# Optimization experiments

Measured on AMD Instinct MI355X. Metric: run time of the kernel, lower is better.

Reference implementation:

```python
import jax, jax.numpy as jnp
import numpy as np

N_NODES = 100000
N_EDGES = 600000
N_GRAPHS = 64
BN_EPS = 1e-5


def setup_inputs() -> dict:
    key = jax.random.key(0)
    ks = jax.random.split(key, 32)
    inp = {
        "x": jax.random.normal(ks[0], (N_NODES, 128), dtype=jnp.float32),
        "edge_index": jax.random.randint(ks[1], (2, N_EDGES), 0, N_NODES, dtype=jnp.int64),
        "batch": jnp.sort(jax.random.randint(ks[2], (N_NODES,), 0, N_GRAPHS, dtype=jnp.int64)),
    }
    dims = [(128, 64, 64), (64, 64, 64), (64, 64, 96)]  # (in, hid, out) per GIN layer
    ki = 3
    for i, (d_in, d_hid, d_out) in enumerate(dims):
        inp[f"l{i}_w1"] = jax.random.normal(ks[ki], (d_in, d_hid), dtype=jnp.float32) * 0.05; ki += 1
        inp[f"l{i}_b1"] = jnp.zeros((d_hid,), dtype=jnp.float32)
        inp[f"l{i}_w2"] = jax.random.normal(ks[ki], (d_hid, d_out), dtype=jnp.float32) * 0.05; ki += 1
        inp[f"l{i}_b2"] = jnp.zeros((d_out,), dtype=jnp.float32)
        inp[f"bn{i}_g"] = jax.random.uniform(ks[ki], (d_out,), minval=0.5, maxval=1.5, dtype=jnp.float32); ki += 1
        inp[f"bn{i}_b"] = jax.random.normal(ks[ki], (d_out,), dtype=jnp.float32) * 0.05; ki += 1
        inp[f"bn{i}_m"] = jax.random.normal(ks[ki], (d_out,), dtype=jnp.float32) * 0.05; ki += 1
        inp[f"bn{i}_v"] = jax.random.uniform(ks[ki], (d_out,), minval=0.5, maxval=1.5, dtype=jnp.float32); ki += 1
    return inp


def _gin_layer(x, src, dst, w1, b1, w2, b2, g, bb, m, v):
    # GINConv (eps=0): h_i = MLP(x_i + sum_{j: j->i} x_j)
    aggr = jax.ops.segment_sum(x[src], dst, num_segments=N_NODES)
    h = x + aggr
    h = jax.nn.relu(h @ w1 + b1) @ w2 + b2
    # eval-mode BatchNorm1d + ReLU
    h = (h - m) * jax.lax.rsqrt(v + BN_EPS) * g + bb
    return jax.nn.relu(h)


def reference(x, edge_index, batch,
              l0_w1, l0_b1, l0_w2, l0_b2, bn0_g, bn0_b, bn0_m, bn0_v,
              l1_w1, l1_b1, l1_w2, l1_b2, bn1_g, bn1_b, bn1_m, bn1_v,
              l2_w1, l2_b1, l2_w2, l2_b2, bn2_g, bn2_b, bn2_m, bn2_v):
    src, dst = edge_index[0], edge_index[1]
    h = _gin_layer(x, src, dst, l0_w1, l0_b1, l0_w2, l0_b2, bn0_g, bn0_b, bn0_m, bn0_v)
    h = _gin_layer(h, src, dst, l1_w1, l1_b1, l1_w2, l1_b2, bn1_g, bn1_b, bn1_m, bn1_v)
    h = _gin_layer(h, src, dst, l2_w1, l2_b1, l2_w2, l2_b2, bn2_g, bn2_b, bn2_m, bn2_v)
    # global mean pool over graphs
    sums = jax.ops.segment_sum(h, batch, num_segments=N_GRAPHS)
    counts = jax.ops.segment_sum(jnp.ones((h.shape[0],), dtype=h.dtype), batch, num_segments=N_GRAPHS)
    return sums / jnp.maximum(counts, 1.0)[:, None]
```

## Files before the change

kernel.cpp:

```cpp
#include <hip/hip_runtime.h>

#define N_NODES 100000
#define N_GRAPHS 64
#define N_EDGES 600000
#define BN_EPS 1e-5f

typedef unsigned short bf16_t;

__device__ __forceinline__ unsigned short f2bf(float f) {
    unsigned int u = __float_as_uint(f);
    u += 0x7FFF + ((u >> 16) & 1);
    return (unsigned short)(u >> 16);
}
__device__ __forceinline__ float4 bf2f4(uint2 p) {
    float4 r;
    r.x = __uint_as_float(p.x << 16);
    r.y = __uint_as_float(p.x & 0xFFFF0000u);
    r.z = __uint_as_float(p.y << 16);
    r.w = __uint_as_float(p.y & 0xFFFF0000u);
    return r;
}
__device__ __forceinline__ uint2 pack4(float a, float b, float c, float d) {
    uint2 p;
    p.x = (unsigned)f2bf(a) | ((unsigned)f2bf(b) << 16);
    p.y = (unsigned)f2bf(c) | ((unsigned)f2bf(d) << 16);
    return p;
}

__global__ void deg_hist_kernel(const int* __restrict__ dst,
                                int* __restrict__ deg, int n_edges) {
    int e = blockIdx.x * blockDim.x + threadIdx.x;
    if (e < n_edges) atomicAdd(&deg[dst[e]], 1);
}

__global__ void scan1_kernel(const int* __restrict__ deg, int* __restrict__ excl,
                             int* __restrict__ partials, int n) {
    __shared__ int s[1024];
    int i = blockIdx.x * 1024 + threadIdx.x;
    int v = (i < n) ? deg[i] : 0;
    s[threadIdx.x] = v;
    __syncthreads();
    for (int off = 1; off < 1024; off <<= 1) {
        int t = (threadIdx.x >= (unsigned)off) ? s[threadIdx.x - off] : 0;
        __syncthreads();
        s[threadIdx.x] += t;
        __syncthreads();
    }
    if (i < n) excl[i] = s[threadIdx.x] - v;
    if (threadIdx.x == 1023) partials[blockIdx.x] = s[1023];
}

__global__ void scan2_kernel(int* partials, int nb) {
    __shared__ int s[128];
    int t = threadIdx.x;
    int v = (t < nb) ? partials[t] : 0;
    s[t] = v;
    __syncthreads();
    for (int off = 1; off < 128; off <<= 1) {
        int u = (t >= off) ? s[t - off] : 0;
        __syncthreads();
        s[t] += u;
        __syncthreads();
    }
    if (t < nb) partials[t] = s[t] - v;
}

__global__ void scan3_kernel(int* __restrict__ rowptr, const int* __restrict__ partials,
                             int n, int total) {
    int i = blockIdx.x * blockDim.x + threadIdx.x;
    if (i < n) rowptr[i] += partials[i >> 10];
    else if (i == n) rowptr[n] = total;
}

__global__ void fill_bounds_kernel(const int* __restrict__ src, const int* __restrict__ dst,
                                   const int* __restrict__ rowptr, int* __restrict__ cursor,
                                   int* __restrict__ eids, const int* __restrict__ batch,
                                   int* __restrict__ gstart, int n_edges, int n_nodes) {
    int e = blockIdx.x * blockDim.x + threadIdx.x;
    if (e < n_edges) {
        int t = dst[e];
        int pos = rowptr[t] + atomicAdd(&cursor[t], 1);
        eids[pos] = src[e];
    }
    if (e < n_nodes) {
        if (e == 0) {
            for (int g = 0; g <= batch[0]; ++g) gstart[g] = 0;
        } else {
            int b0 = batch[e - 1], b1 = batch[e];
            for (int g = b0 + 1; g <= b1; ++g) gstart[g] = e;
        }
        if (e == n_nodes - 1) {
            for (int g = batch[e] + 1; g <= N_GRAPHS; ++g) gstart[g] = n_nodes;
        }
    }
}

struct LayerPrep {
    const float *w1, *w2, *b2, *g, *bb, *m, *v;
    float *w1T, *w2sT, *bias2;
    int DIN, DOUT;
};
struct PrepAll { LayerPrep l[3]; };

__global__ void prep_all_kernel(PrepAll pa, int* __restrict__ deg,
                                int* __restrict__ cursor) {
    LayerPrep P = pa.l[blockIdx.y];
    int i = blockIdx.x * blockDim.x + threadIdx.x;
    if (blockIdx.y == 0) {
        int stride = gridDim.x * blockDim.x;
        for (int k = i; k < N_NODES; k += stride) { deg[k] = 0; cursor[k] = 0; }
    }
    if (i < 64 * P.DIN) {
        int j = i / P.DIN, k = i % P.DIN;
        P.w1T[i] = P.w1[k * 64 + j];
    }
    int i2 = i - 64 * P.DIN;
    if (i2 >= 0 && i2 < P.DOUT * 64) {
        int c = i2 / 64, j = i2 % 64;
        float s = P.g[c] * rsqrtf(P.v[c] + BN_EPS);
        P.w2sT[i2] = P.w2[j * P.DOUT + c] * s;
    }
    int i3 = i2 - P.DOUT * 64;
    if (i3 >= 0 && i3 < P.DOUT) {
        float s = P.g[i3] * rsqrtf(P.v[i3] + BN_EPS);
        P.bias2[i3] = (P.b2[i3] - P.m[i3]) * s + P.bb[i3];
    }
}

__global__ __launch_bounds__(256)
void pre_gemm_kernel(const float* __restrict__ x, const float* __restrict__ w1T,
                     bf16_t* __restrict__ y, int n_nodes) {
    __shared__ float w1s[64 * 128];
    const int tid = threadIdx.x;
    const long base = (long)blockIdx.x * 128;

    const float4* gw1 = (const float4*)w1T;
    for (int i4 = tid; i4 < 16 * 128; i4 += 256) {
        int row = i4 >> 5, k4 = i4 & 31;
        *(float4*)&w1s[row * 128 + ((k4 ^ ((row >> 2) & 7)) << 2)] = gw1[i4];
    }
    __syncthreads();

    const int jg = tid & 15, ng = tid >> 4, xw = jg & 7;
    const float* wp = &w1s[(jg * 4) * 128];
    const float4* xv = (const float4*)x;
    long r[8];
    #pragma unroll
    for (int i = 0; i < 8; ++i) {
        long rr = base + ng * 8 + i;
        r[i] = (rr < n_nodes) ? rr : (n_nodes - 1);
    }
    float acc[8][4] = {};
    #pragma unroll 2
    for (int k4 = 0; k4 < 32; ++k4) {
        const int ko = (k4 ^ xw) << 2;
        float4 w0 = *(const float4*)&wp[0 * 128 + ko];
        float4 w1v = *(const float4*)&wp[1 * 128 + ko];
        float4 w2v = *(const float4*)&wp[2 * 128 + ko];
        float4 w3v = *(const float4*)&wp[3 * 128 + ko];
        #pragma unroll
        for (int i = 0; i < 8; ++i) {
            float4 a = xv[r[i] * 32 + k4];
            acc[i][0] = fmaf(a.x, w0.x, fmaf(a.y, w0.y, fmaf(a.z, w0.z, fmaf(a.w, w0.w, acc[i][0]))));
            acc[i][1] = fmaf(a.x, w1v.x, fmaf(a.y, w1v.y, fmaf(a.z, w1v.z, fmaf(a.w, w1v.w, acc[i][1]))));
            acc[i][2] = fmaf(a.x, w2v.x, fmaf(a.y, w2v.y, fmaf(a.z, w2v.z, fmaf(a.w, w2v.w, acc[i][2]))));
            acc[i][3] = fmaf(a.x, w3v.x, fmaf(a.y, w3v.y, fmaf(a.z, w3v.z, fmaf(a.w, w3v.w, acc[i][3]))));
        }
    }
    #pragma unroll
    for (int i = 0; i < 8; ++i) {
        long n = base + ng * 8 + i;
        if (n < n_nodes) {
            *(uint2*)(y + n * 64 + jg * 4) = pack4(acc[i][0], acc[i][1], acc[i][2], acc[i][3]);
        }
    }
}

__global__ __launch_bounds__(256)
void gather64_kernel(const bf16_t* __restrict__ y, const int* __restrict__ rowptr,
                     const int* __restrict__ eids, const float* __restrict__ b1,
                     float* __restrict__ t, int n_nodes) {
    int node = blockIdx.x * 16 + (threadIdx.x >> 4);
    if (node >= n_nodes) return;
    int f4 = threadIdx.x & 15;
    const uint2* yv = (const uint2*)y;
    float4 acc = bf2f4(yv[(long)node * 16 + f4]);
    int b = rowptr[node], e = rowptr[node + 1];
    int i = b;
    for (; i + 3 < e; i += 4) {
        int s0 = eids[i], s1 = eids[i + 1], s2 = eids[i + 2], s3 = eids[i + 3];
        uint2 q0 = yv[(long)s0 * 16 + f4];
        uint2 q1 = yv[(long)s1 * 16 + f4];
        uint2 q2 = yv[(long)s2 * 16 + f4];
        uint2 q3 = yv[(long)s3 * 16 + f4];
        float4 r0 = bf2f4(q0), r1 = bf2f4(q1), r2 = bf2f4(q2), r3 = bf2f4(q3);
        acc.x += (r0.x + r1.x) + (r2.x + r3.x);
        acc.y += (r0.y + r1.y) + (r2.y + r3.y);
        acc.z += (r0.z + r1.z) + (r2.z + r3.z);
        acc.w += (r0.w + r1.w) + (r2.w + r3.w);
    }
    for (; i < e; ++i) {
        int s = eids[i];
        float4 r = bf2f4(yv[(long)s * 16 + f4]);
        acc.x += r.x; acc.y += r.y; acc.z += r.z; acc.w += r.w;
    }
    float4 bv = ((const float4*)b1)[f4];
    float4 o;
    o.x = fmaxf(acc.x + bv.x, 0.0f);
    o.y = fmaxf(acc.y + bv.y, 0.0f);
    o.z = fmaxf(acc.z + bv.z, 0.0f);
    o.w = fmaxf(acc.w + bv.w, 0.0f);
    ((float4*)t)[(long)node * 16 + f4] = o;
}

__global__ __launch_bounds__(256)
void fused_mid_kernel(const float* __restrict__ t, const float* __restrict__ w2sT,
                      const float* __restrict__ bias2, const float* __restrict__ w1nT,
                      bf16_t* __restrict__ ynext, int n_nodes) {
    constexpr int SS = 68;
    __shared__ float sT[64 * SS];
    __shared__ float wbuf[64 * 64];
    const int tid = threadIdx.x;
    const long base = (long)blockIdx.x * 64;

    const float4* gw2 = (const float4*)w2sT;
    for (int i4 = tid; i4 < 16 * 64; i4 += 256) {
        int row = i4 >> 4, k4 = i4 & 15;
        *(float4*)&wbuf[row * 64 + ((k4 ^ ((row >> 2) & 7)) << 2)] = gw2[i4];
    }
    __syncthreads();

    const int jg = tid & 15, ng = tid >> 4, xw = jg & 7;
    const float4* tv = (const float4*)(t + base * 64);

    float h[4][4];
    {
        const float* wp = &wbuf[(jg * 4) * 64];
        float acc[4][4] = {};
        #pragma unroll 4
        for (int k4 = 0; k4 < 16; ++k4) {
            const int ko = (k4 ^ xw) << 2;
            float4 w0 = *(const float4*)&wp[0 * 64 + ko];
            float4 w1v = *(const float4*)&wp[1 * 64 + ko];
            float4 w2v = *(const float4*)&wp[2 * 64 + ko];
            float4 w3v = *(const float4*)&wp[3 * 64 + ko];
            #pragma unroll
            for (int i = 0; i < 4; ++i) {
                float4 a = tv[(ng * 4 + i) * 16 + k4];
                acc[i][0] = fmaf(a.x, w0.x, fmaf(a.y, w0.y, fmaf(a.z, w0.z, fmaf(a.w, w0.w, acc[i][0]))));
                acc[i][1] = fmaf(a.x, w1v.x, fmaf(a.y, w1v.y, fmaf(a.z, w1v.z, fmaf(a.w, w1v.w, acc[i][1]))));
                acc[i][2] = fmaf(a.x, w2v.x, fmaf(a.y, w2v.y, fmaf(a.z, w2v.z, fmaf(a.w, w2v.w, acc[i][2]))));
                acc[i][3] = fmaf(a.x, w3v.x, fmaf(a.y, w3v.y, fmaf(a.z, w3v.z, fmaf(a.w, w3v.w, acc[i][3]))));
            }
        }
        float4 bv = *(const float4*)&bias2[jg * 4];
        #pragma unroll
        for (int i = 0; i < 4; ++i) {
            h[i][0] = fmaxf(acc[i][0] + bv.x, 0.0f);
            h[i][1] = fmaxf(acc[i][1] + bv.y, 0.0f);
            h[i][2] = fmaxf(acc[i][2] + bv.z, 0.0f);
            h[i][3] = fmaxf(acc[i][3] + bv.w, 0.0f);
        }
    }
    __syncthreads();

    #pragma unroll
    for (int i = 0; i < 4; ++i) {
        float4 hv = {h[i][0], h[i][1], h[i][2], h[i][3]};
        *(float4*)&sT[(ng * 4 + i) * SS + jg * 4] = hv;
    }
    const float4* gw1n = (const float4*)w1nT;
    for (int i4 = tid; i4 < 16 * 64; i4 += 256) {
        int row = i4 >> 4, k4 = i4 & 15;
        *(float4*)&wbuf[row * 64 + ((k4 ^ ((row >> 2) & 7)) << 2)] = gw1n[i4];
    }
    __syncthreads();

    {
        const float* ap = &sT[(ng * 4) * SS];
        const float* wp = &wbuf[(jg * 4) * 64];
        float acc[4][4] = {};
        #pragma unroll 4
        for (int k4 = 0; k4 < 16; ++k4) {
            const int ko = (k4 ^ xw) << 2;
            float4 w0 = *(const float4*)&wp[0 * 64 + ko];
            float4 w1v = *(const float4*)&wp[1 * 64 + ko];
            float4 w2v = *(const float4*)&wp[2 * 64 + ko];
            float4 w3v = *(const float4*)&wp[3 * 64 + ko];
            #pragma unroll
            for (int i = 0; i < 4; ++i) {
                float4 a = *(const float4*)&ap[i * SS + k4 * 4];
                acc[i][0] = fmaf(a.x, w0.x, fmaf(a.y, w0.y, fmaf(a.z, w0.z, fmaf(a.w, w0.w, acc[i][0]))));
                acc[i][1] = fmaf(a.x, w1v.x, fmaf(a.y, w1v.y, fmaf(a.z, w1v.z, fmaf(a.w, w1v.w, acc[i][1]))));
                acc[i][2] = fmaf(a.x, w2v.x, fmaf(a.y, w2v.y, fmaf(a.z, w2v.z, fmaf(a.w, w2v.w, acc[i][2]))));
                acc[i][3] = fmaf(a.x, w3v.x, fmaf(a.y, w3v.y, fmaf(a.z, w3v.z, fmaf(a.w, w3v.w, acc[i][3]))));
            }
        }
        #pragma unroll
        for (int i = 0; i < 4; ++i) {
            long n = base + ng * 4 + i;
            if (n < n_nodes) {
                *(uint2*)(ynext + n * 64 + jg * 4) = pack4(acc[i][0], acc[i][1], acc[i][2], acc[i][3]);
            }
        }
    }
}

__global__ __launch_bounds__(256)
void fused_final_kernel(const float* __restrict__ t, const float* __restrict__ w2sT,
                        const float* __restrict__ bias2, float* __restrict__ out,
                        int n_nodes) {
    constexpr int CPT = 6;
    __shared__ float w2s[96 * 64];
    const int tid = threadIdx.x;
    const long base = (long)blockIdx.x * 64;

    const float4* gw2 = (const float4*)w2sT;
    for (int i4 = tid; i4 < 96 * 16; i4 += 256) {
        int row = i4 >> 4, k4 = i4 & 15;
        *(float4*)&w2s[row * 64 + ((k4 ^ ((row / CPT) & 7)) << 2)] = gw2[i4];
    }
    __syncthreads();

    const int cg_ = tid & 15, ng = tid >> 4, xw = cg_ & 7;
    const float4* tv = (const float4*)(t + base * 64);
    const float* wp = &w2s[(cg_ * CPT) * 64];
    float acc[4][CPT] = {};
    #pragma unroll 4
    for (int k4 = 0; k4 < 16; ++k4) {
        const int ko = (k4 ^ xw) << 2;
        float4 wv[CPT];
        #pragma unroll
        for (int c = 0; c < CPT; ++c) wv[c] = *(const float4*)&wp[c * 64 + ko];
        #pragma unroll
        for (int i = 0; i < 4; ++i) {
            float4 h = tv[(ng * 4 + i) * 16 + k4];
            #pragma unroll
            for (int c = 0; c < CPT; ++c)
                acc[i][c] = fmaf(h.x, wv[c].x, fmaf(h.y, wv[c].y, fmaf(h.z, wv[c].z, fmaf(h.w, wv[c].w, acc[i][c]))));
        }
    }
    float bv[CPT];
    #pragma unroll
    for (int c = 0; c < CPT; ++c) bv[c] = bias2[cg_ * CPT + c];
    #pragma unroll
    for (int i = 0; i < 4; ++i) {
        long n = base + ng * 4 + i;
        if (n < n_nodes) {
            float* op = out + n * 96 + cg_ * CPT;
            #pragma unroll
            for (int c = 0; c < CPT; ++c) op[c] = fmaxf(acc[i][c] + bv[c], 0.0f);
        }
    }
}

#define POOL_SPLIT 16
__global__ __launch_bounds__(192)
void pool_seg_kernel(const float* __restrict__ h, const int* __restrict__ gstart,
                     float* __restrict__ part) {
    int g = blockIdx.x >> 4;
    int s = blockIdx.x & 15;
    int lo = gstart[g], hi = gstart[g + 1];
    int len = hi - lo;
    int seg = (len + POOL_SPLIT - 1) / POOL_SPLIT;
    int a = lo + s * seg;
    int b = a + seg; if (b > hi) b = hi;

    int f4 = threadIdx.x % 24;
    int chain = threadIdx.x / 24;
    const float4* hv = (const float4*)h;
    float4 acc = {0.0f, 0.0f, 0.0f, 0.0f};
    for (int n = a + chain; n < b; n += 8) {
        float4 v = hv[(long)n * 24 + f4];
        acc.x += v.x; acc.y += v.y; acc.z += v.z; acc.w += v.w;
    }
    __shared__ float4 red[8][24];
    red[chain][f4] = acc;
    __syncthreads();
    if (threadIdx.x < 24) {
        float4 t = red[0][threadIdx.x];
        #pragma unroll
        for (int c = 1; c < 8; ++c) {
            float4 r = red[c][threadIdx.x];
            t.x += r.x; t.y += r.y; t.z += r.z; t.w += r.w;
        }
        *(float4*)&part[((long)blockIdx.x) * 96 + threadIdx.x * 4] = t;
    }
}

__global__ void finalize_kernel(const float* __restrict__ part,
                                const int* __restrict__ gstart,
                                float* __restrict__ out) {
    int i = blockIdx.x * blockDim.x + threadIdx.x;
    if (i >= N_GRAPHS * 96) return;
    int g = i / 96, c = i - g * 96;
    float s = 0.0f;
    #pragma unroll
    for (int k = 0; k < POOL_SPLIT; ++k) s += part[((long)g * POOL_SPLIT + k) * 96 + c];
    float cnt = (float)(gstart[g + 1] - gstart[g]);
    out[i] = s / fmaxf(cnt, 1.0f);
}

static inline int cdiv_l(long a, int b) { return (int)((a + b - 1) / b); }

extern "C" void kernel_launch(void* const* d_in, const int* in_sizes, int n_in,
                              void* d_out, int out_size, void* d_ws, size_t ws_size,
                              hipStream_t stream) {
    const float* x     = (const float*)d_in[0];
    const int*   ei    = (const int*)d_in[1];
    const int*   src   = ei;
    const int*   dst   = ei + N_EDGES;
    const int*   batch = (const int*)d_in[2];

    const float* P[3][8];
    int p = 3;
    for (int l = 0; l < 3; ++l)
        for (int q = 0; q < 8; ++q)
            P[l][q] = (const float*)d_in[p++];

    const long NP = N_NODES + 128;
    char* wsb   = (char*)d_ws;
    bf16_t* yA  = (bf16_t*)wsb;
    bf16_t* yB  = yA + NP * 64;
    float* gB   = (float*)(yB + NP * 64);
    float* h2   = gB + NP * 64;
    float* q    = h2 + NP * 96;
    float* w1T[3], *w2sT[3], *bias2[3];
    for (int l = 0; l < 3; ++l) {
        w1T[l] = q;   q += 64 * 128;
        w2sT[l] = q;  q += 96 * 64;
        bias2[l] = q; q += 96;
    }
    float* part   = q;
    int* gstart   = (int*)(part + N_GRAPHS * POOL_SPLIT * 96);
    int* deg      = gstart + 72;
    int* cursor   = deg + N_NODES;
    int* partials = cursor + N_NODES;
    int* rowptr   = partials + 128;
    int* eids     = rowptr + (N_NODES + 1);

    const int B = 256;
    const int DIN[3]  = {128, 64, 64};
    const int DOUT[3] = {64, 64, 96};

    PrepAll pa;
    for (int l = 0; l < 3; ++l) {
        pa.l[l].w1 = P[l][0]; pa.l[l].w2 = P[l][2]; pa.l[l].b2 = P[l][3];
        pa.l[l].g = P[l][4];  pa.l[l].bb = P[l][5]; pa.l[l].m = P[l][6];
        pa.l[l].v = P[l][7];
        pa.l[l].w1T = w1T[l]; pa.l[l].w2sT = w2sT[l]; pa.l[l].bias2 = bias2[l];
        pa.l[l].DIN = DIN[l]; pa.l[l].DOUT = DOUT[l];
    }
    dim3 pgrid(cdiv_l(64 * 128 + 96 * 64 + 96, B), 3);
    prep_all_kernel<<<pgrid, B, 0, stream>>>(pa, deg, cursor);

    deg_hist_kernel<<<cdiv_l(N_EDGES, B), B, 0, stream>>>(dst, deg, N_EDGES);
    int nblk = cdiv_l(N_NODES, 1024);
    scan1_kernel<<<nblk, 1024, 0, stream>>>(deg, rowptr, partials, N_NODES);
    scan2_kernel<<<1, 128, 0, stream>>>(partials, nblk);
    scan3_kernel<<<cdiv_l(N_NODES + 1, B), B, 0, stream>>>(rowptr, partials, N_NODES, N_EDGES);
    fill_bounds_kernel<<<cdiv_l(N_EDGES, B), B, 0, stream>>>(
        src, dst, rowptr, cursor, eids, batch, gstart, N_EDGES, N_NODES);

    const int ntiles = cdiv_l(N_NODES, 64);
    const int ngather = cdiv_l(N_NODES, 16);

    pre_gemm_kernel<<<cdiv_l(N_NODES, 128), 256, 0, stream>>>(x, w1T[0], yA, N_NODES);
    gather64_kernel<<<ngather, 256, 0, stream>>>(yA, rowptr, eids, P[0][1], gB, N_NODES);
    fused_mid_kernel<<<ntiles, 256, 0, stream>>>(
        gB, w2sT[0], bias2[0], w1T[1], yB, N_NODES);
    gather64_kernel<<<ngather, 256, 0, stream>>>(yB, rowptr, eids, P[1][1], gB, N_NODES);
    fused_mid_kernel<<<ntiles, 256, 0, stream>>>(
        gB, w2sT[1], bias2[1], w1T[2], yA, N_NODES);
    gather64_kernel<<<ngather, 256, 0, stream>>>(yA, rowptr, eids, P[2][1], gB, N_NODES);
    fused_final_kernel<<<ntiles, 256, 0, stream>>>(
        gB, w2sT[2], bias2[2], h2, N_NODES);

    pool_seg_kernel<<<N_GRAPHS * POOL_SPLIT, 192, 0, stream>>>(h2, gstart, part);
    finalize_kernel<<<cdiv_l(N_GRAPHS * 96, B), B, 0, stream>>>(
        part, gstart, (float*)d_out);
}
```

Baseline: 396.3 us.

## Fuse neighbor gather into per-layer MLP kernels via shared-memory tiles

Removes the standalone gather kernels. Each fused MLP kernel now aggregates its 64-node tile's neighbor features straight into shared memory, then runs the GEMMs from there. This drops the fp32 intermediate buffer write and read and three kernel launches per forward. The trade-off is that each block does irregular gather work before its GEMM, so per-block latency and load imbalance rise. The first pre-GEMM also shrinks to 64 rows per block, giving more blocks.

After: 406.0 us. 1.02x slower.

```diff
diff --git a/kernel.cpp b/kernel.cpp
--- a/kernel.cpp
+++ b/kernel.cpp
@@ -132,7 +132,7 @@
                      bf16_t* __restrict__ y, int n_nodes) {
     __shared__ float w1s[64 * 128];
     const int tid = threadIdx.x;
-    const long base = (long)blockIdx.x * 128;
+    const long base = (long)blockIdx.x * 64;
 
     const float4* gw1 = (const float4*)w1T;
     for (int i4 = tid; i4 < 16 * 128; i4 += 256) {
@@ -144,14 +144,14 @@
     const int jg = tid & 15, ng = tid >> 4, xw = jg & 7;
     const float* wp = &w1s[(jg * 4) * 128];
     const float4* xv = (const float4*)x;
-    long r[8];
-    #pragma unroll
-    for (int i = 0; i < 8; ++i) {
-        long rr = base + ng * 8 + i;
+    long r[4];
+    #pragma unroll
+    for (int i = 0; i < 4; ++i) {
+        long rr = base + ng * 4 + i;
         r[i] = (rr < n_nodes) ? rr : (n_nodes - 1);
     }
-    float acc[8][4] = {};
-    #pragma unroll 2
+    float acc[4][4] = {};
+    #pragma unroll 4
     for (int k4 = 0; k4 < 32; ++k4) {
         const int ko = (k4 ^ xw) << 2;
         float4 w0 = *(const float4*)&wp[0 * 128 + ko];
@@ -159,7 +159,7 @@
         float4 w2v = *(const float4*)&wp[2 * 128 + ko];
         float4 w3v = *(const float4*)&wp[3 * 128 + ko];
         #pragma unroll
-        for (int i = 0; i < 8; ++i) {
+        for (int i = 0; i < 4; ++i) {
             float4 a = xv[r[i] * 32 + k4];
             acc[i][0] = fmaf(a.x, w0.x, fmaf(a.y, w0.y, fmaf(a.z, w0.z, fmaf(a.w, w0.w, acc[i][0]))));
             acc[i][1] = fmaf(a.x, w1v.x, fmaf(a.y, w1v.y, fmaf(a.z, w1v.z, fmaf(a.w, w1v.w, acc[i][1]))));
@@ -168,56 +168,67 @@
         }
     }
     #pragma unroll
-    for (int i = 0; i < 8; ++i) {
-        long n = base + ng * 8 + i;
+    for (int i = 0; i < 4; ++i) {
+        long n = base + ng * 4 + i;
         if (n < n_nodes) {
             *(uint2*)(y + n * 64 + jg * 4) = pack4(acc[i][0], acc[i][1], acc[i][2], acc[i][3]);
         }
     }
 }
 
+#define SS 68
+__device__ __forceinline__ void gather_tile_lds(const bf16_t* __restrict__ y,
+                                                const int* __restrict__ rowptr,
+                                                const int* __restrict__ eids,
+                                                const float* __restrict__ b1,
+                                                float* sT, long base, int n_nodes,
+                                                int tid) {
+    const uint2* yv = (const uint2*)y;
+    const int f4 = tid & 15;
+    const int gidx = tid >> 4;
+    const float4 bv = ((const float4*)b1)[f4];
+    #pragma unroll
+    for (int pass = 0; pass < 4; ++pass) {
+        int nl = pass * 16 + gidx;
+        long node = base + nl;
+        float4 acc = {0.0f, 0.0f, 0.0f, 0.0f};
+        if (node < n_nodes) {
+            acc = bf2f4(yv[node * 16 + f4]);
+            int b = rowptr[node], e = rowptr[node + 1];
+            int i = b;
+            for (; i + 3 < e; i += 4) {
+                int s0 = eids[i], s1 = eids[i + 1], s2 = eids[i + 2], s3 = eids[i + 3];
+                uint2 q0 = yv[(long)s0 * 16 + f4];
+                uint2 q1 = yv[(long)s1 * 16 + f4];
+                uint2 q2 = yv[(long)s2 * 16 + f4];
+                uint2 q3 = yv[(long)s3 * 16 + f4];
+                float4 r0 = bf2f4(q0), r1 = bf2f4(q1), r2 = bf2f4(q2), r3 = bf2f4(q3);
+                acc.x += (r0.x + r1.x) + (r2.x + r3.x);
+                acc.y += (r0.y + r1.y) + (r2.y + r3.y);
+                acc.z += (r0.z + r1.z) + (r2.z + r3.z);
+                acc.w += (r0.w + r1.w) + (r2.w + r3.w);
+            }
+            for (; i < e; ++i) {
+                int s = eids[i];
+                float4 r = bf2f4(yv[(long)s * 16 + f4]);
+                acc.x += r.x; acc.y += r.y; acc.z += r.z; acc.w += r.w;
+            }
+        }
+        float4 o;
+        o.x = fmaxf(acc.x + bv.x, 0.0f);
+        o.y = fmaxf(acc.y + bv.y, 0.0f);
+        o.z = fmaxf(acc.z + bv.z, 0.0f);
+        o.w = fmaxf(acc.w + bv.w, 0.0f);
+        *(float4*)&sT[nl * SS + f4 * 4] = o;
+    }
+}
+
 __global__ __launch_bounds__(256)
-void gather64_kernel(const bf16_t* __restrict__ y, const int* __restrict__ rowptr,
-                     const int* __restrict__ eids, const float* __restrict__ b1,
-                     float* __restrict__ t, int n_nodes) {
-    int node = blockIdx.x * 16 + (threadIdx.x >> 4);
-    if (node >= n_nodes) return;
-    int f4 = threadIdx.x & 15;
-    const uint2* yv = (const uint2*)y;
-    float4 acc = bf2f4(yv[(long)node * 16 + f4]);
-    int b = rowptr[node], e = rowptr[node + 1];
-    int i = b;
-    for (; i + 3 < e; i += 4) {
-        int s0 = eids[i], s1 = eids[i + 1], s2 = eids[i + 2], s3 = eids[i + 3];
-        uint2 q0 = yv[(long)s0 * 16 + f4];
-        uint2 q1 = yv[(long)s1 * 16 + f4];
-        uint2 q2 = yv[(long)s2 * 16 + f4];
-        uint2 q3 = yv[(long)s3 * 16 + f4];
-        float4 r0 = bf2f4(q0), r1 = bf2f4(q1), r2 = bf2f4(q2), r3 = bf2f4(q3);
-        acc.x += (r0.x + r1.x) + (r2.x + r3.x);
-        acc.y += (r0.y + r1.y) + (r2.y + r3.y);
-        acc.z += (r0.z + r1.z) + (r2.z + r3.z);
-        acc.w += (r0.w + r1.w) + (r2.w + r3.w);
-    }
-    for (; i < e; ++i) {
-        int s = eids[i];
-        float4 r = bf2f4(yv[(long)s * 16 + f4]);
-        acc.x += r.x; acc.y += r.y; acc.z += r.z; acc.w += r.w;
-    }
-    float4 bv = ((const float4*)b1)[f4];
-    float4 o;
-    o.x = fmaxf(acc.x + bv.x, 0.0f);
-    o.y = fmaxf(acc.y + bv.y, 0.0f);
-    o.z = fmaxf(acc.z + bv.z, 0.0f);
-    o.w = fmaxf(acc.w + bv.w, 0.0f);
-    ((float4*)t)[(long)node * 16 + f4] = o;
-}
-
-__global__ __launch_bounds__(256)
-void fused_mid_kernel(const float* __restrict__ t, const float* __restrict__ w2sT,
-                      const float* __restrict__ bias2, const float* __restrict__ w1nT,
-                      bf16_t* __restrict__ ynext, int n_nodes) {
-    constexpr int SS = 68;
+void fused_mid_kernel(const bf16_t* __restrict__ y, const int* __restrict__ rowptr,
+                      const int* __restrict__ eids, const float* __restrict__ b1,
+                      const float* __restrict__ w2sT, const float* __restrict__ bias2,
+                      const float* __restrict__ w1nT, bf16_t* __restrict__ ynext,
+                      int n_nodes) {
     __shared__ float sT[64 * SS];
     __shared__ float wbuf[64 * 64];
     const int tid = threadIdx.x;
@@ -228,54 +239,12 @@
         int row = i4 >> 4, k4 = i4 & 15;
         *(float4*)&wbuf[row * 64 + ((k4 ^ ((row >> 2) & 7)) << 2)] = gw2[i4];
     }
+    gather_tile_lds(y, rowptr, eids, b1, sT, base, n_nodes, tid);
     __syncthreads();
 
     const int jg = tid & 15, ng = tid >> 4, xw = jg & 7;
-    const float4* tv = (const float4*)(t + base * 64);
 
     float h[4][4];
-    {
-        const float* wp = &wbuf[(jg * 4) * 64];
-        float acc[4][4] = {};
-        #pragma unroll 4
-        for (int k4 = 0; k4 < 16; ++k4) {
-            const int ko = (k4 ^ xw) << 2;
-            float4 w0 = *(const float4*)&wp[0 * 64 + ko];
-            float4 w1v = *(const float4*)&wp[1 * 64 + ko];
-            float4 w2v = *(const float4*)&wp[2 * 64 + ko];
-            float4 w3v = *(const float4*)&wp[3 * 64 + ko];
-            #pragma unroll
-            for (int i = 0; i < 4; ++i) {
-                float4 a = tv[(ng * 4 + i) * 16 + k4];
-                acc[i][0] = fmaf(a.x, w0.x, fmaf(a.y, w0.y, fmaf(a.z, w0.z, fmaf(a.w, w0.w, acc[i][0]))));
-                acc[i][1] = fmaf(a.x, w1v.x, fmaf(a.y, w1v.y, fmaf(a.z, w1v.z, fmaf(a.w, w1v.w, acc[i][1]))));
-                acc[i][2] = fmaf(a.x, w2v.x, fmaf(a.y, w2v.y, fmaf(a.z, w2v.z, fmaf(a.w, w2v.w, acc[i][2]))));
-                acc[i][3] = fmaf(a.x, w3v.x, fmaf(a.y, w3v.y, fmaf(a.z, w3v.z, fmaf(a.w, w3v.w, acc[i][3]))));
-            }
-        }
-        float4 bv = *(const float4*)&bias2[jg * 4];
-        #pragma unroll
-        for (int i = 0; i < 4; ++i) {
-            h[i][0] = fmaxf(acc[i][0] + bv.x, 0.0f);
-            h[i][1] = fmaxf(acc[i][1] + bv.y, 0.0f);
-            h[i][2] = fmaxf(acc[i][2] + bv.z, 0.0f);
-            h[i][3] = fmaxf(acc[i][3] + bv.w, 0.0f);
-        }
-    }
-    __syncthreads();
-
-    #pragma unroll
-    for (int i = 0; i < 4; ++i) {
-        float4 hv = {h[i][0], h[i][1], h[i][2], h[i][3]};
-        *(float4*)&sT[(ng * 4 + i) * SS + jg * 4] = hv;
-    }
-    const float4* gw1n = (const float4*)w1nT;
-    for (int i4 = tid; i4 < 16 * 64; i4 += 256) {
-        int row = i4 >> 4, k4 = i4 & 15;
-        *(float4*)&wbuf[row * 64 + ((k4 ^ ((row >> 2) & 7)) << 2)] = gw1n[i4];
-    }
-    __syncthreads();
-
     {
         const float* ap = &sT[(ng * 4) * SS];
         const float* wp = &wbuf[(jg * 4) * 64];
@@ -296,6 +265,49 @@
                 acc[i][3] = fmaf(a.x, w3v.x, fmaf(a.y, w3v.y, fmaf(a.z, w3v.z, fmaf(a.w, w3v.w, acc[i][3]))));
             }
         }
+        float4 bv = *(const float4*)&bias2[jg * 4];
+        #pragma unroll
+        for (int i = 0; i < 4; ++i) {
+            h[i][0] = fmaxf(acc[i][0] + bv.x, 0.0f);
+            h[i][1] = fmaxf(acc[i][1] + bv.y, 0.0f);
+            h[i][2] = fmaxf(acc[i][2] + bv.z, 0.0f);
+            h[i][3] = fmaxf(acc[i][3] + bv.w, 0.0f);
+        }
+    }
+    __syncthreads();
+
+    #pragma unroll
+    for (int i = 0; i < 4; ++i) {
+        float4 hv = {h[i][0], h[i][1], h[i][2], h[i][3]};
+        *(float4*)&sT[(ng * 4 + i) * SS + jg * 4] = hv;
+    }
+    const float4* gw1n = (const float4*)w1nT;
+    for (int i4 = tid; i4 < 16 * 64; i4 += 256) {
+        int row = i4 >> 4, k4 = i4 & 15;
+        *(float4*)&wbuf[row * 64 + ((k4 ^ ((row >> 2) & 7)) << 2)] = gw1n[i4];
+    }
+    __syncthreads();
+
+    {
+        const float* ap = &sT[(ng * 4) * SS];
+        const float* wp = &wbuf[(jg * 4) * 64];
+        float acc[4][4] = {};
+        #pragma unroll 4
+        for (int k4 = 0; k4 < 16; ++k4) {
+            const int ko = (k4 ^ xw) << 2;
+            float4 w0 = *(const float4*)&wp[0 * 64 + ko];
+            float4 w1v = *(const float4*)&wp[1 * 64 + ko];
+            float4 w2v = *(const float4*)&wp[2 * 64 + ko];
+            float4 w3v = *(const float4*)&wp[3 * 64 + ko];
+            #pragma unroll
+            for (int i = 0; i < 4; ++i) {
+                float4 a = *(const float4*)&ap[i * SS + k4 * 4];
+                acc[i][0] = fmaf(a.x, w0.x, fmaf(a.y, w0.y, fmaf(a.z, w0.z, fmaf(a.w, w0.w, acc[i][0]))));
+                acc[i][1] = fmaf(a.x, w1v.x, fmaf(a.y, w1v.y, fmaf(a.z, w1v.z, fmaf(a.w, w1v.w, acc[i][1]))));
+                acc[i][2] = fmaf(a.x, w2v.x, fmaf(a.y, w2v.y, fmaf(a.z, w2v.z, fmaf(a.w, w2v.w, acc[i][2]))));
+                acc[i][3] = fmaf(a.x, w3v.x, fmaf(a.y, w3v.y, fmaf(a.z, w3v.z, fmaf(a.w, w3v.w, acc[i][3]))));
+            }
+        }
         #pragma unroll
         for (int i = 0; i < 4; ++i) {
             long n = base + ng * 4 + i;
@@ -307,10 +319,12 @@
 }
 
 __global__ __launch_bounds__(256)
-void fused_final_kernel(const float* __restrict__ t, const float* __restrict__ w2sT,
-                        const float* __restrict__ bias2, float* __restrict__ out,
-                        int n_nodes) {
+void fused_final_kernel(const bf16_t* __restrict__ y, const int* __restrict__ rowptr,
+                        const int* __restrict__ eids, const float* __restrict__ b1,
+                        const float* __restrict__ w2sT, const float* __restrict__ bias2,
+                        float* __restrict__ out, int n_nodes) {
     constexpr int CPT = 6;
+    __shared__ float sT[64 * SS];
     __shared__ float w2s[96 * 64];
     const int tid = threadIdx.x;
     const long base = (long)blockIdx.x * 64;
@@ -320,10 +334,11 @@
         int row = i4 >> 4, k4 = i4 & 15;
         *(float4*)&w2s[row * 64 + ((k4 ^ ((row / CPT) & 7)) << 2)] = gw2[i4];
     }
+    gather_tile_lds(y, rowptr, eids, b1, sT, base, n_nodes, tid);
     __syncthreads();
 
     const int cg_ = tid & 15, ng = tid >> 4, xw = cg_ & 7;
-    const float4* tv = (const float4*)(t + base * 64);
+    const float* hp = &sT[(ng * 4) * SS];
     const float* wp = &w2s[(cg_ * CPT) * 64];
     float acc[4][CPT] = {};
     #pragma unroll 4
@@ -334,7 +349,7 @@
         for (int c = 0; c < CPT; ++c) wv[c] = *(const float4*)&wp[c * 64 + ko];
         #pragma unroll
         for (int i = 0; i < 4; ++i) {
-            float4 h = tv[(ng * 4 + i) * 16 + k4];
+            float4 h = *(const float4*)&hp[i * SS + k4 * 4];
             #pragma unroll
             for (int c = 0; c < CPT; ++c)
                 acc[i][c] = fmaf(h.x, wv[c].x, fmaf(h.y, wv[c].y, fmaf(h.z, wv[c].z, fmaf(h.w, wv[c].w, acc[i][c]))));
@@ -422,8 +437,7 @@
     char* wsb   = (char*)d_ws;
     bf16_t* yA  = (bf16_t*)wsb;
     bf16_t* yB  = yA + NP * 64;
-    float* gB   = (float*)(yB + NP * 64);
-    float* h2   = gB + NP * 64;
+    float* h2   = (float*)(yB + NP * 64);
     float* q    = h2 + NP * 96;
     float* w1T[3], *w2sT[3], *bias2[3];
     for (int l = 0; l < 3; ++l) {
@@ -463,18 +477,14 @@
         src, dst, rowptr, cursor, eids, batch, gstart, N_EDGES, N_NODES);
 
     const int ntiles = cdiv_l(N_NODES, 64);
-    const int ngather = cdiv_l(N_NODES, 16);
-
-    pre_gemm_kernel<<<cdiv_l(N_NODES, 128), 256, 0, stream>>>(x, w1T[0], yA, N_NODES);
-    gather64_kernel<<<ngather, 256, 0, stream>>>(yA, rowptr, eids, P[0][1], gB, N_NODES);
+
+    pre_gemm_kernel<<<ntiles, 256, 0, stream>>>(x, w1T[0], yA, N_NODES);
     fused_mid_kernel<<<ntiles, 256, 0, stream>>>(
-        gB, w2sT[0], bias2[0], w1T[1], yB, N_NODES);
-    gather64_kernel<<<ngather, 256, 0, stream>>>(yB, rowptr, eids, P[1][1], gB, N_NODES);
+        yA, rowptr, eids, P[0][1], w2sT[0], bias2[0], w1T[1], yB, N_NODES);
     fused_mid_kernel<<<ntiles, 256, 0, stream>>>(
-        gB, w2sT[1], bias2[1], w1T[2], yA, N_NODES);
-    gather64_kernel<<<ngather, 256, 0, stream>>>(yA, rowptr, eids, P[2][1], gB, N_NODES);
+        yB, rowptr, eids, P[1][1], w2sT[1], bias2[1], w1T[2], yA, N_NODES);
     fused_final_kernel<<<ntiles, 256, 0, stream>>>(
-        gB, w2sT[2], bias2[2], h2, N_NODES);
+        yA, rowptr, eids, P[2][1], w2sT[2], bias2[2], h2, N_NODES);
 
     pool_seg_kernel<<<N_GRAPHS * POOL_SPLIT, 192, 0, stream>>>(h2, gstart, part);
     finalize_kernel<<<cdiv_l(N_GRAPHS * 96, B), B, 0, stream>>>(
```
